# Kernel tuning notes

Measured on AMD Instinct MI355X. Metric: run time of the kernel, lower is better.

The kernel has to match this reference:

```python
import jax, jax.numpy as jnp
import numpy as np
from jax import lax

N_FFT = 1024
HOP = 256
FFT_BIN = N_FFT // 2 + 1  # 513


def make_stft_kernel(n_fft: int) -> jnp.ndarray:
    """Fixed DFT basis kernel, shape (2*fft_bin, 1, n_fft), windowed with periodic Hann."""
    fft_bin = n_fft // 2 + 1
    # torch.linspace(0, 1, n_fft) is endpoint-inclusive, same as jnp.linspace
    t = jnp.linspace(0.0, 1.0, n_fft, dtype=jnp.float32)[None, None, :]
    k = jnp.arange(fft_bin, dtype=jnp.float32)[:, None, None]
    xt = t * k * (2.0 * jnp.pi)
    kernel = jnp.concatenate([jnp.cos(xt), jnp.sin(xt)], axis=0)  # (2*fft_bin, 1, n_fft)
    # torch.hann_window is periodic: 0.5*(1 - cos(2*pi*n/N))
    n = jnp.arange(n_fft, dtype=jnp.float32)
    hann = 0.5 * (1.0 - jnp.cos(2.0 * jnp.pi * n / n_fft))
    return kernel * hann[None, None, :]


def setup_inputs() -> dict:
    key = jax.random.key(0)
    x = jax.random.normal(key, (16, 1, 262144), dtype=jnp.float32)
    kernel = make_stft_kernel(N_FFT)
    return {"x": x, "kernel": kernel}


def reference(x, kernel):
    # padding == 'center'
    left = N_FFT // 2
    right = N_FFT - left
    x = jnp.pad(x, ((0, 0), (0, 0), (left, right)))
    # strided conv1d with fixed DFT-basis kernel
    y = lax.conv_general_dilated(
        x, kernel,
        window_strides=(HOP,),
        padding='VALID',
        dimension_numbers=('NCW', 'OIW', 'NCW'),
    )  # (B, 2*fft_bin, num_frames)
    real, imag = jnp.split(y, 2, axis=1)
    return real, imag
```

## Files before the change

kernel.cpp:

```cpp
#include <hip/hip_runtime.h>
#include <hip/hip_bf16.h>

#define NFFT    1024
#define HOPSZ   256
#define XLEN    262144
#define PADLEN  (XLEN + NFFT)
#define NBATCH  16
#define NBINS2  1026
#define FBIN    513
#define NFRAMES 1025
#define NGF     (NBATCH * NFRAMES)
#define TOTOUT  ((size_t)NBATCH * FBIN * NFRAMES)

#define KT 64
#define NKT 16
#define NT_TILES 64
#define MT_TILES 4
#define NWG (MT_TILES * NT_TILES)
#define ABYTES 32768
#define BUFE   32768
#define BUFB   65536
#define NTAIL  49184
#define PSTRIDE 132
#define LDS_BYTES (256 * PSTRIDE * 4)

typedef short bf16x8 __attribute__((ext_vector_type(8)));
typedef float f32x4  __attribute__((ext_vector_type(4)));
typedef unsigned short u16x8 __attribute__((ext_vector_type(8)));
typedef unsigned short u16x4 __attribute__((ext_vector_type(4)));

__device__ __forceinline__ unsigned short f2bf(float f) {
  union { float f; unsigned u; } v; v.f = f;
  unsigned r = v.u + 0x7fffu + ((v.u >> 16) & 1u);
  return (unsigned short)(r >> 16);
}
__device__ __forceinline__ float bf2f(unsigned short h) {
  union { unsigned u; float f; } v; v.u = ((unsigned)h) << 16; return v.f;
}

typedef __attribute__((address_space(1))) void void_g;
typedef __attribute__((address_space(3))) void void_l;
__device__ __forceinline__ void gload_lds16(const void* g, void* l) {
  __builtin_amdgcn_global_load_lds((void_g*)(g), (void_l*)(l), 16, 0, 0);
}

__global__ __launch_bounds__(256) void pack_x_kernel(const float* __restrict__ x,
                                                     unsigned short* __restrict__ xp) {
  long long t = (long long)blockIdx.x * 256 + threadIdx.x;
  long long base = t * 8;
  if (base >= (long long)NBATCH * PADLEN) return;
  int b   = (int)(base / PADLEN);
  int pos = (int)(base % PADLEN);
  const float* xb = x + (long long)b * XLEN;
  u16x8 v;
#pragma unroll
  for (int j = 0; j < 8; ++j) {
    int xi = pos + j - (NFFT / 2);
    float f = ((unsigned)xi < (unsigned)XLEN) ? xb[xi] : 0.0f;
    v[j] = f2bf(f);
  }
  *reinterpret_cast<u16x8*>(xp + base) = v;
}

__global__ __launch_bounds__(256) void pack_w_kernel(const float* __restrict__ W,
                                                     unsigned short* __restrict__ Wb) {
  long long t = ((long long)blockIdx.x * 256 + threadIdx.x) * 4;
  if (t >= (long long)NBINS2 * NFFT) return;
  float4 f = *reinterpret_cast<const float4*>(W + t);
  u16x4 v;
  v[0] = f2bf(f.x); v[1] = f2bf(f.y); v[2] = f2bf(f.z); v[3] = f2bf(f.w);
  *reinterpret_cast<u16x4*>(Wb + t) = v;
}

__global__ __launch_bounds__(512, 2) void stft_mfma8_kernel(const unsigned short* __restrict__ Xp,
                                                            const unsigned short* __restrict__ Wb,
                                                            float* __restrict__ out) {
  extern __shared__ unsigned short lds[];
  const int tid = threadIdx.x;
  const int l   = tid & 63;
  const int w   = tid >> 6;
  const int wr  = w >> 2;
  const int wc  = w & 3;
  const int r16 = l & 15, hi = l >> 4;

  const int bid = blockIdx.x;
  const int c_  = bid >> 3;
  const int nt  = (bid & 7) * 8 + (c_ & 7);
  const int mt  = c_ >> 3;
  const int bin0 = mt * 256;
  const int gf0  = nt * 256;

  const int lr = l >> 3;
  const int ls = l & 7;
  const int cswz = ((ls ^ lr) << 3);

  unsigned aqoff[4];
#pragma unroll
  for (int qi = 0; qi < 4; ++qi)
    aqoff[qi] = (unsigned)(bin0 + qi * 64 + w * 8 + lr) * NFFT + cswz;
  unsigned boff[4];
#pragma unroll
  for (int j = 0; j < 4; ++j) {
    const int gf = gf0 + (w * 4 + j) * 8 + lr;
    const int bb = gf / NFRAMES;
    const int fr = gf - bb * NFRAMES;
    boff[j] = (unsigned)bb * PADLEN + (unsigned)fr * HOPSZ + cswz;
  }

#define STAGE(D, KC) do { \
    _Pragma("unroll") \
    for (int q_ = 0; q_ < 4; ++q_) \
      gload_lds16(Wb + aqoff[q_] + (KC), lds + (D) * BUFE + q_ * 4096 + w * 512); \
    _Pragma("unroll") \
    for (int j_ = 0; j_ < 4; ++j_) \
      gload_lds16(Xp + boff[j_] + (KC), lds + (D) * BUFE + 16384 + (w * 4 + j_) * 512); \
    } while (0)

  const int aB0 = (wr * 128 + r16) * 128;
  const int bB0 = ABYTES + (wc * 64 + r16) * 128;
  const int swz = (r16 & 7) << 4;
  const int c0  = (hi * 16) ^ swz;
  const int c1  = (64 + hi * 16) ^ swz;

#define RD12(BASE, C, AARR, BARR) do { \
    _Pragma("unroll") \
    for (int n_ = 0; n_ < 4; ++n_) \
      BARR[n_] = *reinterpret_cast<const bf16x8*>((const char*)(BASE) + bB0 + n_ * 2048 + (C)); \
    _Pragma("unroll") \
    for (int m_ = 0; m_ < 8; ++m_) \
      AARR[m_] = *reinterpret_cast<const bf16x8*>((const char*)(BASE) + aB0 + m_ * 2048 + (C)); \
    } while (0)

#define MFMA32(AARR, BARR) do { \
    __builtin_amdgcn_s_setprio(1); \
    _Pragma("unroll") \
    for (int m_ = 0; m_ < 8; ++m_) { \
      _Pragma("unroll") \
      for (int n_ = 0; n_ < 4; ++n_) \
        acc[m_][n_] = __builtin_amdgcn_mfma_f32_16x16x32_bf16(AARR[m_], BARR[n_], acc[m_][n_], 0, 0, 0); \
    } \
    __builtin_amdgcn_s_setprio(0); } while (0)

  f32x4 acc[8][4] = {};
  bf16x8 A0[8], B0[4], A1[8], B1[4];

  STAGE(0, 0);
  STAGE(1, KT);
  asm volatile("s_waitcnt vmcnt(8)" ::: "memory");
  __builtin_amdgcn_s_barrier();
  __builtin_amdgcn_sched_barrier(0);
  RD12(lds, c0, A0, B0);

  for (int t = 0; t < NKT; ++t) {
    const int ci = t & 1;
    const char* cbuf = (const char*)lds + ci * BUFB;
    const char* nbuf = (const char*)lds + (ci ^ 1) * BUFB;
    const int kc2 = (t + 2) << 6;

    RD12(cbuf, c1, A1, B1);
    __builtin_amdgcn_sched_barrier(0);
    asm volatile("s_waitcnt lgkmcnt(12)" ::: "memory");
    __builtin_amdgcn_sched_barrier(0);
    MFMA32(A0, B0);

    asm volatile("s_waitcnt vmcnt(0) lgkmcnt(0)" ::: "memory");
    __builtin_amdgcn_sched_barrier(0);
    __builtin_amdgcn_s_barrier();
    __builtin_amdgcn_sched_barrier(0);
    if (t < NKT - 1) RD12(nbuf, c0, A0, B0);
    if (t < NKT - 2) STAGE(ci, kc2);
    __builtin_amdgcn_sched_barrier(0);
    MFMA32(A1, B1);
  }

  {
    float* patch = (float*)lds;
    const int col     = l & 15;
    const int rbase   = (l >> 4) * 4;
    const int h_mine  = wc >> 1;
    const int colbase = (wc & 1) * 64;

#pragma unroll
    for (int h = 0; h < 2; ++h) {
      __builtin_amdgcn_s_barrier();
      if (h_mine == h) {
#pragma unroll
        for (int m = 0; m < 8; ++m)
#pragma unroll
          for (int n2 = 0; n2 < 4; ++n2)
#pragma unroll
            for (int r = 0; r < 4; ++r)
              patch[(wr * 128 + m * 16 + rbase + r) * PSTRIDE + colbase + n2 * 16 + col] =
                  acc[m][n2][r];
      }
      __builtin_amdgcn_s_barrier();

      size_t baseR[2];
      int cols[2];
#pragma unroll
      for (int j = 0; j < 2; ++j) {
        const int gf = gf0 + h * 128 + j * 64 + l;
        const int bb = gf / NFRAMES;
        const int fr = gf - bb * NFRAMES;
        baseR[j] = (size_t)bb * FBIN * NFRAMES + fr;
        cols[j]  = j * 64 + l;
      }
      for (int i = 0; i < 32; ++i) {
        const int row = i * 8 + w;
        const int bin = bin0 + row;
        const size_t binoff = (size_t)bin * NFRAMES;
#pragma unroll
        for (int j = 0; j < 2; ++j) {
          const float v = patch[row * PSTRIDE + cols[j]];
          size_t off = binoff + (bin < FBIN ? baseR[j]
                                            : baseR[j] + TOTOUT - (size_t)FBIN * NFRAMES);
          out[off] = v;
        }
      }
    }
  }
#undef STAGE
#undef RD12
#undef MFMA32
}

__global__ __launch_bounds__(512) void stft_tail_kernel(const unsigned short* __restrict__ Xp,
                                                        const unsigned short* __restrict__ Wb,
                                                        float* __restrict__ out) {
  const int wid = (int)((blockIdx.x * 512 + threadIdx.x) >> 6);
  const int l   = threadIdx.x & 63;
  if (wid >= NTAIL) return;
  int bin, gf;
  if (wid < 2 * NGF) { bin = 1024 + (wid & 1); gf = wid >> 1; }
  else { const int s = wid - 2 * NGF; gf = 16384 + (s & 15); bin = s >> 4; }
  const int bb = gf / NFRAMES;
  const int fr = gf - bb * NFRAMES;
  const unsigned short* xr = Xp + (size_t)bb * PADLEN + (size_t)fr * HOPSZ + l * 16;
  const unsigned short* wr = Wb + (size_t)bin * NFFT + l * 16;
  u16x8 x0 = *reinterpret_cast<const u16x8*>(xr);
  u16x8 x1 = *reinterpret_cast<const u16x8*>(xr + 8);
  u16x8 w0 = *reinterpret_cast<const u16x8*>(wr);
  u16x8 w1 = *reinterpret_cast<const u16x8*>(wr + 8);
  float s0 = 0.f, s1 = 0.f;
#pragma unroll
  for (int j = 0; j < 8; ++j) {
    s0 = fmaf(bf2f(x0[j]), bf2f(w0[j]), s0);
    s1 = fmaf(bf2f(x1[j]), bf2f(w1[j]), s1);
  }
  float s = s0 + s1;
#pragma unroll
  for (int k = 32; k >= 1; k >>= 1) s += __shfl_xor(s, k);
  if (l == 0) {
    size_t off;
    if (bin < FBIN) off = ((size_t)bb * FBIN + bin) * NFRAMES + fr;
    else            off = TOTOUT + ((size_t)bb * FBIN + (bin - FBIN)) * NFRAMES + fr;
    out[off] = s;
  }
}

__global__ void stft_direct_kernel(const float* __restrict__ x, const float* __restrict__ W,
                                   float* __restrict__ out,
                                   int bin_lo, int nbins, int fr_lo, int nframes) {
  long long total = (long long)NBATCH * nbins * nframes;
  for (long long t = (long long)blockIdx.x * blockDim.x + threadIdx.x; t < total;
       t += (long long)gridDim.x * blockDim.x) {
    int fr = fr_lo + (int)(t % nframes);
    long long q = t / nframes;
    int bin = bin_lo + (int)(q % nbins);
    int b   = (int)(q / nbins);
    const float* xb = x + (long long)b * XLEN;
    const float* wrow = W + (long long)bin * NFFT;
    float s = 0.f;
    const int base = fr * HOPSZ - (NFFT / 2);
    for (int j = 0; j < NFFT; ++j) {
      int xi = base + j;
      float xv = ((unsigned)xi < (unsigned)XLEN) ? xb[xi] : 0.f;
      s = fmaf(xv, wrow[j], s);
    }
    size_t off;
    if (bin < FBIN) off = ((size_t)b * FBIN + bin) * NFRAMES + fr;
    else            off = TOTOUT + ((size_t)b * FBIN + (bin - FBIN)) * NFRAMES + fr;
    out[off] = s;
  }
}

extern "C" void kernel_launch(void* const* d_in, const int* in_sizes, int n_in,
                              void* d_out, int out_size, void* d_ws, size_t ws_size,
                              hipStream_t stream) {
  const float* x = (const float*)d_in[0];
  const float* W = (const float*)d_in[1];
  float* out = (float*)d_out;

  const size_t xp_bytes = (size_t)NBATCH * PADLEN * sizeof(unsigned short);
  const size_t wb_bytes = (size_t)NBINS2 * NFFT * sizeof(unsigned short);

  if (ws_size >= xp_bytes + wb_bytes) {
    unsigned short* xp = (unsigned short*)d_ws;
    unsigned short* wb = (unsigned short*)((char*)d_ws + xp_bytes);

    {
      long long threads = (long long)NBATCH * PADLEN / 8;
      pack_x_kernel<<<(int)((threads + 255) / 256), 256, 0, stream>>>(x, xp);
    }
    pack_w_kernel<<<(NBINS2 * NFFT / 4 + 255) / 256, 256, 0, stream>>>(W, wb);

    stft_mfma8_kernel<<<NWG, 512, LDS_BYTES, stream>>>(xp, wb, out);
    stft_tail_kernel<<<NTAIL / 8, 512, 0, stream>>>(xp, wb, out);
  } else {
    stft_direct_kernel<<<2048, 256, 0, stream>>>(x, W, out, 0, NBINS2, 0, NFRAMES);
  }
}
```

Baseline: 69.39 us.

## Restructure GEMM main loop into quadrant-wise LDS reads and MFMA phases

Replaces the two-half K-split software pipeline (RD12/MFMA32 with depth-2 prefetch) with a four-phase quadrant schedule. Each phase reads only the A or B fragments it needs and issues 16 MFMAs on one 4x2 accumulator quadrant, with workgroup barriers between phases. Global prefetch depth drops from two stages ahead to one, and the loop is no longer unrolled. The aim is to interleave LDS reads with MFMA work across waves, HipKittens-style, and to lower register pressure. The extra barriers and shallower prefetch may expose more global-load latency.

```diff
diff --git a/kernel.cpp b/kernel.cpp
--- a/kernel.cpp
+++ b/kernel.cpp
@@ -122,55 +122,80 @@
   const int c0  = (hi * 16) ^ swz;
   const int c1  = (64 + hi * 16) ^ swz;
 
-#define RD12(BASE, C, AARR, BARR) do { \
-    _Pragma("unroll") \
-    for (int n_ = 0; n_ < 4; ++n_) \
-      BARR[n_] = *reinterpret_cast<const bf16x8*>((const char*)(BASE) + bB0 + n_ * 2048 + (C)); \
-    _Pragma("unroll") \
-    for (int m_ = 0; m_ < 8; ++m_) \
-      AARR[m_] = *reinterpret_cast<const bf16x8*>((const char*)(BASE) + aB0 + m_ * 2048 + (C)); \
-    } while (0)
-
-#define MFMA32(AARR, BARR) do { \
+#define RD_A(CB, MH, AARR) do { \
+    _Pragma("unroll") \
+    for (int m_ = 0; m_ < 4; ++m_) { \
+      AARR[m_ * 2 + 0] = *reinterpret_cast<const bf16x8*>((CB) + aB0 + ((MH) * 4 + m_) * 2048 + c0); \
+      AARR[m_ * 2 + 1] = *reinterpret_cast<const bf16x8*>((CB) + aB0 + ((MH) * 4 + m_) * 2048 + c1); \
+    } } while (0)
+#define RD_B(CB, NH, BARR) do { \
+    _Pragma("unroll") \
+    for (int n_ = 0; n_ < 2; ++n_) { \
+      BARR[n_ * 2 + 0] = *reinterpret_cast<const bf16x8*>((CB) + bB0 + ((NH) * 2 + n_) * 2048 + c0); \
+      BARR[n_ * 2 + 1] = *reinterpret_cast<const bf16x8*>((CB) + bB0 + ((NH) * 2 + n_) * 2048 + c1); \
+    } } while (0)
+
+#define MFMA_Q(AARR, BARR, MH, NH) do { \
     __builtin_amdgcn_s_setprio(1); \
     _Pragma("unroll") \
-    for (int m_ = 0; m_ < 8; ++m_) { \
+    for (int m_ = 0; m_ < 4; ++m_) { \
       _Pragma("unroll") \
-      for (int n_ = 0; n_ < 4; ++n_) \
-        acc[m_][n_] = __builtin_amdgcn_mfma_f32_16x16x32_bf16(AARR[m_], BARR[n_], acc[m_][n_], 0, 0, 0); \
+      for (int n_ = 0; n_ < 2; ++n_) { \
+        acc[(MH) * 4 + m_][(NH) * 2 + n_] = __builtin_amdgcn_mfma_f32_16x16x32_bf16( \
+            AARR[m_ * 2 + 0], BARR[n_ * 2 + 0], acc[(MH) * 4 + m_][(NH) * 2 + n_], 0, 0, 0); \
+        acc[(MH) * 4 + m_][(NH) * 2 + n_] = __builtin_amdgcn_mfma_f32_16x16x32_bf16( \
+            AARR[m_ * 2 + 1], BARR[n_ * 2 + 1], acc[(MH) * 4 + m_][(NH) * 2 + n_], 0, 0, 0); \
+      } \
     } \
     __builtin_amdgcn_s_setprio(0); } while (0)
 
+#define LGKM0  asm volatile("s_waitcnt lgkmcnt(0)" ::: "memory"); __builtin_amdgcn_sched_barrier(0)
+#define SBAR   __builtin_amdgcn_s_barrier()
+#define SCHED0 __builtin_amdgcn_sched_barrier(0)
+
   f32x4 acc[8][4] = {};
-  bf16x8 A0[8], B0[4], A1[8], B1[4];
+  bf16x8 Am0[8], Am1[8], Bn0[4], Bn1[4];
 
   STAGE(0, 0);
-  STAGE(1, KT);
-  asm volatile("s_waitcnt vmcnt(8)" ::: "memory");
-  __builtin_amdgcn_s_barrier();
-  __builtin_amdgcn_sched_barrier(0);
-  RD12(lds, c0, A0, B0);
-
+  asm volatile("s_waitcnt vmcnt(0)" ::: "memory");
+  SCHED0;
+  SBAR;
+  SCHED0;
+
+#pragma unroll 1
   for (int t = 0; t < NKT; ++t) {
-    const int ci = t & 1;
-    const char* cbuf = (const char*)lds + ci * BUFB;
-    const char* nbuf = (const char*)lds + (ci ^ 1) * BUFB;
-    const int kc2 = (t + 2) << 6;
-
-    RD12(cbuf, c1, A1, B1);
-    __builtin_amdgcn_sched_barrier(0);
-    asm volatile("s_waitcnt lgkmcnt(12)" ::: "memory");
-    __builtin_amdgcn_sched_barrier(0);
-    MFMA32(A0, B0);
-
-    asm volatile("s_waitcnt vmcnt(0) lgkmcnt(0)" ::: "memory");
-    __builtin_amdgcn_sched_barrier(0);
-    __builtin_amdgcn_s_barrier();
-    __builtin_amdgcn_sched_barrier(0);
-    if (t < NKT - 1) RD12(nbuf, c0, A0, B0);
-    if (t < NKT - 2) STAGE(ci, kc2);
-    __builtin_amdgcn_sched_barrier(0);
-    MFMA32(A1, B1);
+    const char* cbuf = (const char*)lds + (t & 1) * BUFB;
+    const int kc1 = (t + 1) << 6;
+
+    RD_A(cbuf, 0, Am0);
+    RD_B(cbuf, 0, Bn0);
+    SCHED0;
+    if (t < NKT - 1) STAGE((t & 1) ^ 1, kc1);
+    SBAR;
+    LGKM0;
+    MFMA_Q(Am0, Bn0, 0, 0);
+    SBAR;
+
+    RD_A(cbuf, 1, Am1);
+    SCHED0;
+    SBAR;
+    LGKM0;
+    MFMA_Q(Am1, Bn0, 1, 0);
+    SBAR;
+
+    RD_B(cbuf, 1, Bn1);
+    SCHED0;
+    SBAR;
+    LGKM0;
+    MFMA_Q(Am1, Bn1, 1, 1);
+    SBAR;
+
+    MFMA_Q(Am0, Bn1, 0, 1);
+    if (t < NKT - 1) {
+      asm volatile("s_waitcnt vmcnt(0)" ::: "memory");
+      SCHED0;
+    }
+    SBAR;
   }
 
   {
@@ -182,7 +207,7 @@
 
 #pragma unroll
     for (int h = 0; h < 2; ++h) {
-      __builtin_amdgcn_s_barrier();
+      SBAR;
       if (h_mine == h) {
 #pragma unroll
         for (int m = 0; m < 8; ++m)
@@ -193,7 +218,7 @@
               patch[(wr * 128 + m * 16 + rbase + r) * PSTRIDE + colbase + n2 * 16 + col] =
                   acc[m][n2][r];
       }
-      __builtin_amdgcn_s_barrier();
+      SBAR;
 
       size_t baseR[2];
       int cols[2];
@@ -220,8 +245,12 @@
     }
   }
 #undef STAGE
-#undef RD12
-#undef MFMA32
+#undef RD_A
+#undef RD_B
+#undef MFMA_Q
+#undef LGKM0
+#undef SBAR
+#undef SCHED0
 }
 
 __global__ __launch_bounds__(512) void stft_tail_kernel(const unsigned short* __restrict__ Xp,
```

Result: slower. 72.81 us (+4.9%).

## Fuse pack and tail kernels into one prep launch, store MFMA results directly

Applied to the files above, without the earlier changes.

Merges the x/W bf16 packing kernels and the tail-bin kernel into a single prep kernel. The tail part now reads fp32 inputs directly, so it no longer waits on the packed buffers, and launch count drops from four to two. The MFMA kernel swaps operand roles so each accumulator's four lanes map to consecutive frames. Each thread then writes a 4-wide vector straight to global memory, removing the LDS transpose staging and its barriers. The tail now uses fp32 rather than bf16 math, and the direct stores have less coalescing across lanes than the old row-wise writes.

```diff
diff --git a/kernel.cpp b/kernel.cpp
--- a/kernel.cpp
+++ b/kernel.cpp
@@ -21,11 +21,16 @@
 #define BUFE   32768
 #define BUFB   65536
 #define NTAIL  49184
-#define PSTRIDE 132
-#define LDS_BYTES (256 * PSTRIDE * 4)
+#define LDS_BYTES (2 * BUFB)
+
+#define PX_BLKS 2056
+#define PW_BLKS 1026
+#define TL_BLKS 12296
+#define PREP_BLKS (PX_BLKS + PW_BLKS + TL_BLKS)
 
 typedef short bf16x8 __attribute__((ext_vector_type(8)));
 typedef float f32x4  __attribute__((ext_vector_type(4)));
+typedef float f32x4u __attribute__((ext_vector_type(4), aligned(4)));
 typedef unsigned short u16x8 __attribute__((ext_vector_type(8)));
 typedef unsigned short u16x4 __attribute__((ext_vector_type(4)));
 
@@ -34,9 +39,6 @@
   unsigned r = v.u + 0x7fffu + ((v.u >> 16) & 1u);
   return (unsigned short)(r >> 16);
 }
-__device__ __forceinline__ float bf2f(unsigned short h) {
-  union { unsigned u; float f; } v; v.u = ((unsigned)h) << 16; return v.f;
-}
 
 typedef __attribute__((address_space(1))) void void_g;
 typedef __attribute__((address_space(3))) void void_l;
@@ -44,32 +46,74 @@
   __builtin_amdgcn_global_load_lds((void_g*)(g), (void_l*)(l), 16, 0, 0);
 }
 
-__global__ __launch_bounds__(256) void pack_x_kernel(const float* __restrict__ x,
-                                                     unsigned short* __restrict__ xp) {
-  long long t = (long long)blockIdx.x * 256 + threadIdx.x;
-  long long base = t * 8;
-  if (base >= (long long)NBATCH * PADLEN) return;
-  int b   = (int)(base / PADLEN);
-  int pos = (int)(base % PADLEN);
-  const float* xb = x + (long long)b * XLEN;
-  u16x8 v;
-#pragma unroll
-  for (int j = 0; j < 8; ++j) {
-    int xi = pos + j - (NFFT / 2);
-    float f = ((unsigned)xi < (unsigned)XLEN) ? xb[xi] : 0.0f;
-    v[j] = f2bf(f);
-  }
-  *reinterpret_cast<u16x8*>(xp + base) = v;
-}
-
-__global__ __launch_bounds__(256) void pack_w_kernel(const float* __restrict__ W,
-                                                     unsigned short* __restrict__ Wb) {
-  long long t = ((long long)blockIdx.x * 256 + threadIdx.x) * 4;
-  if (t >= (long long)NBINS2 * NFFT) return;
-  float4 f = *reinterpret_cast<const float4*>(W + t);
-  u16x4 v;
-  v[0] = f2bf(f.x); v[1] = f2bf(f.y); v[2] = f2bf(f.z); v[3] = f2bf(f.w);
-  *reinterpret_cast<u16x4*>(Wb + t) = v;
+__global__ __launch_bounds__(256) void prep_kernel(const float* __restrict__ x,
+                                                   const float* __restrict__ W,
+                                                   unsigned short* __restrict__ xp,
+                                                   unsigned short* __restrict__ wb,
+                                                   float* __restrict__ out) {
+  const int bid = blockIdx.x;
+  const int tid = threadIdx.x;
+
+  if (bid < PX_BLKS) {
+    long long base = ((long long)bid * 256 + tid) * 8;
+    int b   = (int)(base / PADLEN);
+    int pos = (int)(base % PADLEN);
+    const float* xb = x + (long long)b * XLEN;
+    u16x8 v;
+#pragma unroll
+    for (int j = 0; j < 8; ++j) {
+      int xi = pos + j - (NFFT / 2);
+      float f = ((unsigned)xi < (unsigned)XLEN) ? xb[xi] : 0.0f;
+      v[j] = f2bf(f);
+    }
+    *reinterpret_cast<u16x8*>(xp + base) = v;
+    return;
+  }
+  if (bid < PX_BLKS + PW_BLKS) {
+    long long t = (((long long)(bid - PX_BLKS)) * 256 + tid) * 4;
+    float4 f = *reinterpret_cast<const float4*>(W + t);
+    u16x4 v;
+    v[0] = f2bf(f.x); v[1] = f2bf(f.y); v[2] = f2bf(f.z); v[3] = f2bf(f.w);
+    *reinterpret_cast<u16x4*>(wb + t) = v;
+    return;
+  }
+  {
+    const int wid = (bid - PX_BLKS - PW_BLKS) * 4 + (tid >> 6);
+    const int l   = tid & 63;
+    int bin, gf;
+    if (wid < 2 * NGF) { bin = 1024 + (wid & 1); gf = wid >> 1; }
+    else { const int s = wid - 2 * NGF; gf = 16384 + (s & 15); bin = s >> 4; }
+    const int bb = gf / NFRAMES;
+    const int fr = gf - bb * NFRAMES;
+    const float* xb = x + (size_t)bb * XLEN;
+    const float* wrow = W + (size_t)bin * NFFT + l * 16;
+    const int base = fr * HOPSZ - (NFFT / 2) + l * 16;
+    float s0 = 0.f;
+    if (fr >= 2 && fr <= 1022) {
+#pragma unroll
+      for (int q = 0; q < 4; ++q) {
+        float4 xv = *reinterpret_cast<const float4*>(xb + base + q * 4);
+        float4 wv = *reinterpret_cast<const float4*>(wrow + q * 4);
+        s0 = fmaf(xv.x, wv.x, s0); s0 = fmaf(xv.y, wv.y, s0);
+        s0 = fmaf(xv.z, wv.z, s0); s0 = fmaf(xv.w, wv.w, s0);
+      }
+    } else {
+#pragma unroll
+      for (int j = 0; j < 16; ++j) {
+        int xi = base + j;
+        float xv = ((unsigned)xi < (unsigned)XLEN) ? xb[xi] : 0.f;
+        s0 = fmaf(xv, wrow[j], s0);
+      }
+    }
+#pragma unroll
+    for (int k = 32; k >= 1; k >>= 1) s0 += __shfl_xor(s0, k);
+    if (l == 0) {
+      size_t off;
+      if (bin < FBIN) off = ((size_t)bb * FBIN + bin) * NFRAMES + fr;
+      else            off = TOTOUT + ((size_t)bb * FBIN + (bin - FBIN)) * NFRAMES + fr;
+      out[off] = s0;
+    }
+  }
 }
 
 __global__ __launch_bounds__(512, 2) void stft_mfma8_kernel(const unsigned short* __restrict__ Xp,
@@ -116,105 +160,91 @@
       gload_lds16(Xp + boff[j_] + (KC), lds + (D) * BUFE + 16384 + (w * 4 + j_) * 512); \
     } while (0)
 
-  const int aB0 = (wr * 128 + r16) * 128;
-  const int bB0 = ABYTES + (wc * 64 + r16) * 128;
+  const int xB0 = ABYTES + (wr * 128 + r16) * 128;
+  const int wB0 = (wc * 64 + r16) * 128;
   const int swz = (r16 & 7) << 4;
   const int c0  = (hi * 16) ^ swz;
   const int c1  = (64 + hi * 16) ^ swz;
 
-#define RD12(BASE, C, AARR, BARR) do { \
+#define RD12(BASE, C, XARR, WARR) do { \
     _Pragma("unroll") \
     for (int n_ = 0; n_ < 4; ++n_) \
-      BARR[n_] = *reinterpret_cast<const bf16x8*>((const char*)(BASE) + bB0 + n_ * 2048 + (C)); \
+      WARR[n_] = *reinterpret_cast<const bf16x8*>((const char*)(BASE) + wB0 + n_ * 2048 + (C)); \
     _Pragma("unroll") \
     for (int m_ = 0; m_ < 8; ++m_) \
-      AARR[m_] = *reinterpret_cast<const bf16x8*>((const char*)(BASE) + aB0 + m_ * 2048 + (C)); \
+      XARR[m_] = *reinterpret_cast<const bf16x8*>((const char*)(BASE) + xB0 + m_ * 2048 + (C)); \
     } while (0)
 
-#define MFMA32(AARR, BARR) do { \
+#define MFMA32(XARR, WARR) do { \
     __builtin_amdgcn_s_setprio(1); \
     _Pragma("unroll") \
     for (int m_ = 0; m_ < 8; ++m_) { \
       _Pragma("unroll") \
       for (int n_ = 0; n_ < 4; ++n_) \
-        acc[m_][n_] = __builtin_amdgcn_mfma_f32_16x16x32_bf16(AARR[m_], BARR[n_], acc[m_][n_], 0, 0, 0); \
+        acc[m_][n_] = __builtin_amdgcn_mfma_f32_16x16x32_bf16(XARR[m_], WARR[n_], acc[m_][n_], 0, 0, 0); \
     } \
     __builtin_amdgcn_s_setprio(0); } while (0)
 
   f32x4 acc[8][4] = {};
-  bf16x8 A0[8], B0[4], A1[8], B1[4];
+  bf16x8 X0[8], W0[4], X1[8], W1[4];
 
   STAGE(0, 0);
   STAGE(1, KT);
   asm volatile("s_waitcnt vmcnt(8)" ::: "memory");
   __builtin_amdgcn_s_barrier();
   __builtin_amdgcn_sched_barrier(0);
-  RD12(lds, c0, A0, B0);
-
+  RD12(lds, c0, X0, W0);
+
+#pragma unroll 1
   for (int t = 0; t < NKT; ++t) {
     const int ci = t & 1;
     const char* cbuf = (const char*)lds + ci * BUFB;
     const char* nbuf = (const char*)lds + (ci ^ 1) * BUFB;
     const int kc2 = (t + 2) << 6;
 
-    RD12(cbuf, c1, A1, B1);
+    RD12(cbuf, c1, X1, W1);
     __builtin_amdgcn_sched_barrier(0);
     asm volatile("s_waitcnt lgkmcnt(12)" ::: "memory");
     __builtin_amdgcn_sched_barrier(0);
-    MFMA32(A0, B0);
+    MFMA32(X0, W0);
 
     asm volatile("s_waitcnt vmcnt(0) lgkmcnt(0)" ::: "memory");
     __builtin_amdgcn_sched_barrier(0);
     __builtin_amdgcn_s_barrier();
     __builtin_amdgcn_sched_barrier(0);
-    if (t < NKT - 1) RD12(nbuf, c0, A0, B0);
+    if (t < NKT - 1) RD12(nbuf, c0, X0, W0);
     if (t < NKT - 2) STAGE(ci, kc2);
     __builtin_amdgcn_sched_barrier(0);
-    MFMA32(A1, B1);
+    MFMA32(X1, W1);
   }
 
   {
-    float* patch = (float*)lds;
-    const int col     = l & 15;
-    const int rbase   = (l >> 4) * 4;
-    const int h_mine  = wc >> 1;
-    const int colbase = (wc & 1) * 64;
-
-#pragma unroll
-    for (int h = 0; h < 2; ++h) {
-      __builtin_amdgcn_s_barrier();
-      if (h_mine == h) {
-#pragma unroll
-        for (int m = 0; m < 8; ++m)
-#pragma unroll
-          for (int n2 = 0; n2 < 4; ++n2)
-#pragma unroll
-            for (int r = 0; r < 4; ++r)
-              patch[(wr * 128 + m * 16 + rbase + r) * PSTRIDE + colbase + n2 * 16 + col] =
-                  acc[m][n2][r];
-      }
-      __builtin_amdgcn_s_barrier();
-
-      size_t baseR[2];
-      int cols[2];
-#pragma unroll
-      for (int j = 0; j < 2; ++j) {
-        const int gf = gf0 + h * 128 + j * 64 + l;
-        const int bb = gf / NFRAMES;
-        const int fr = gf - bb * NFRAMES;
-        baseR[j] = (size_t)bb * FBIN * NFRAMES + fr;
-        cols[j]  = j * 64 + l;
-      }
-      for (int i = 0; i < 32; ++i) {
-        const int row = i * 8 + w;
-        const int bin = bin0 + row;
-        const size_t binoff = (size_t)bin * NFRAMES;
-#pragma unroll
-        for (int j = 0; j < 2; ++j) {
-          const float v = patch[row * PSTRIDE + cols[j]];
-          size_t off = binoff + (bin < FBIN ? baseR[j]
-                                            : baseR[j] + TOTOUT - (size_t)FBIN * NFRAMES);
-          out[off] = v;
+    const int bcol  = l & 15;
+    const int fquad = (l >> 4) * 4;
+#pragma unroll
+    for (int mf = 0; mf < 8; ++mf) {
+      const int gf = gf0 + wr * 128 + mf * 16 + fquad;
+      const int bb = gf / NFRAMES;
+      const int fr = gf - bb * NFRAMES;
+#pragma unroll
+      for (int nb = 0; nb < 4; ++nb) {
+        const int bin = bin0 + wc * 64 + nb * 16 + bcol;
+        if (fr <= NFRAMES - 4) {
+          size_t rowbase;
+          if (bin < FBIN) rowbase = ((size_t)bb * FBIN + bin) * NFRAMES;
+          else            rowbase = TOTOUT + ((size_t)bb * FBIN + (bin - FBIN)) * NFRAMES;
+          *reinterpret_cast<f32x4u*>(out + rowbase + fr) = acc[mf][nb];
+        } else {
+#pragma unroll
+          for (int r = 0; r < 4; ++r) {
+            const int gfr = gf + r;
+            const int bbr = gfr / NFRAMES;
+            const int frr = gfr - bbr * NFRAMES;
+            size_t rb;
+            if (bin < FBIN) rb = ((size_t)bbr * FBIN + bin) * NFRAMES;
+            else            rb = TOTOUT + ((size_t)bbr * FBIN + (bin - FBIN)) * NFRAMES;
+            out[rb + frr] = acc[mf][nb][r];
+          }
         }
       }
     }
@@ -222,40 +252,6 @@
 #undef STAGE
 #undef RD12
 #undef MFMA32
-}
-
-__global__ __launch_bounds__(512) void stft_tail_kernel(const unsigned short* __restrict__ Xp,
-                                                        const unsigned short* __restrict__ Wb,
-                                                        float* __restrict__ out) {
-  const int wid = (int)((blockIdx.x * 512 + threadIdx.x) >> 6);
-  const int l   = threadIdx.x & 63;
-  if (wid >= NTAIL) return;
-  int bin, gf;
-  if (wid < 2 * NGF) { bin = 1024 + (wid & 1); gf = wid >> 1; }
-  else { const int s = wid - 2 * NGF; gf = 16384 + (s & 15); bin = s >> 4; }
-  const int bb = gf / NFRAMES;
-  const int fr = gf - bb * NFRAMES;
-  const unsigned short* xr = Xp + (size_t)bb * PADLEN + (size_t)fr * HOPSZ + l * 16;
-  const unsigned short* wr = Wb + (size_t)bin * NFFT + l * 16;
-  u16x8 x0 = *reinterpret_cast<const u16x8*>(xr);
-  u16x8 x1 = *reinterpret_cast<const u16x8*>(xr + 8);
-  u16x8 w0 = *reinterpret_cast<const u16x8*>(wr);
-  u16x8 w1 = *reinterpret_cast<const u16x8*>(wr + 8);
-  float s0 = 0.f, s1 = 0.f;
-#pragma unroll
-  for (int j = 0; j < 8; ++j) {
-    s0 = fmaf(bf2f(x0[j]), bf2f(w0[j]), s0);
-    s1 = fmaf(bf2f(x1[j]), bf2f(w1[j]), s1);
-  }
-  float s = s0 + s1;
-#pragma unroll
-  for (int k = 32; k >= 1; k >>= 1) s += __shfl_xor(s, k);
-  if (l == 0) {
-    size_t off;
-    if (bin < FBIN) off = ((size_t)bb * FBIN + bin) * NFRAMES + fr;
-    else            off = TOTOUT + ((size_t)bb * FBIN + (bin - FBIN)) * NFRAMES + fr;
-    out[off] = s;
-  }
 }
 
 __global__ void stft_direct_kernel(const float* __restrict__ x, const float* __restrict__ W,
@@ -298,14 +294,8 @@
     unsigned short* xp = (unsigned short*)d_ws;
     unsigned short* wb = (unsigned short*)((char*)d_ws + xp_bytes);
 
-    {
-      long long threads = (long long)NBATCH * PADLEN / 8;
-      pack_x_kernel<<<(int)((threads + 255) / 256), 256, 0, stream>>>(x, xp);
-    }
-    pack_w_kernel<<<(NBINS2 * NFFT / 4 + 255) / 256, 256, 0, stream>>>(W, wb);
-
+    prep_kernel<<<PREP_BLKS, 256, 0, stream>>>(x, W, xp, wb, out);
     stft_mfma8_kernel<<<NWG, 512, LDS_BYTES, stream>>>(xp, wb, out);
-    stft_tail_kernel<<<NTAIL / 8, 512, 0, stream>>>(xp, wb, out);
   } else {
     stft_direct_kernel<<<2048, 256, 0, stream>>>(x, W, out, 0, NBINS2, 0, NFRAMES);
   }
```

After: 95.96 us. +38.3%, slower.

## Retile STFT GEMM to 256x128 tiles with 4 waves and triple-buffered K=32 staging

Applied to the files above, without the earlier changes.

Replaces the 8-wave 256x256-tile GEMM kernel with a 4-wave 256x128-tile kernel. It stages K in chunks of 32 through a three-deep LDS ring, so one barrier per step overlaps loads with MFMA work. The frame-major epilogue now writes two adjacent frames per lane as 8-byte stores, with special handling where a pair crosses a batch boundary. The aim is to double the workgroup count, improve occupancy, shrink LDS use and widen output stores, at the cost of less data reuse per tile and more K iterations.

```diff
diff --git a/kernel.cpp b/kernel.cpp
--- a/kernel.cpp
+++ b/kernel.cpp
@@ -12,20 +12,18 @@
 #define NGF     (NBATCH * NFRAMES)
 #define TOTOUT  ((size_t)NBATCH * FBIN * NFRAMES)
 
-#define KT 64
-#define NKT 16
-#define NT_TILES 64
-#define MT_TILES 4
-#define NWG (MT_TILES * NT_TILES)
-#define ABYTES 32768
-#define BUFE   32768
-#define BUFB   65536
+#define KT 32
+#define NKT 32
+#define NWG 512
+#define BUFE 12288
+#define BUFB 24576
+#define LDS_BYTES (3 * BUFB)
 #define NTAIL  49184
 #define PSTRIDE 132
-#define LDS_BYTES (256 * PSTRIDE * 4)
 
 typedef short bf16x8 __attribute__((ext_vector_type(8)));
 typedef float f32x4  __attribute__((ext_vector_type(4)));
+typedef float f32x2u __attribute__((ext_vector_type(2), aligned(4)));
 typedef unsigned short u16x8 __attribute__((ext_vector_type(8)));
 typedef unsigned short u16x4 __attribute__((ext_vector_type(4)));
 
@@ -72,149 +70,153 @@
   *reinterpret_cast<u16x4*>(Wb + t) = v;
 }
 
-__global__ __launch_bounds__(512, 2) void stft_mfma8_kernel(const unsigned short* __restrict__ Xp,
+__global__ __launch_bounds__(256, 2) void stft_mfma4_kernel(const unsigned short* __restrict__ Xp,
                                                             const unsigned short* __restrict__ Wb,
                                                             float* __restrict__ out) {
   extern __shared__ unsigned short lds[];
   const int tid = threadIdx.x;
   const int l   = tid & 63;
   const int w   = tid >> 6;
-  const int wr  = w >> 2;
-  const int wc  = w & 3;
   const int r16 = l & 15, hi = l >> 4;
 
-  const int bid = blockIdx.x;
-  const int c_  = bid >> 3;
-  const int nt  = (bid & 7) * 8 + (c_ & 7);
-  const int mt  = c_ >> 3;
+  const int bid  = blockIdx.x;
+  const int wgid = (bid & 7) * 64 + (bid >> 3);
+  const int mt   = wgid >> 7;
+  const int nt   = wgid & 127;
   const int bin0 = mt * 256;
-  const int gf0  = nt * 256;
-
-  const int lr = l >> 3;
-  const int ls = l & 7;
-  const int cswz = ((ls ^ lr) << 3);
+  const int gf0  = nt * 128;
+
+  const int lr = l >> 2;
+  const int ls = l & 3;
+  const int gsw = (lr >> 1) & 3;
+  const int cswz = ((ls ^ gsw) << 3);
 
   unsigned aqoff[4];
 #pragma unroll
-  for (int qi = 0; qi < 4; ++qi)
-    aqoff[qi] = (unsigned)(bin0 + qi * 64 + w * 8 + lr) * NFFT + cswz;
-  unsigned boff[4];
-#pragma unroll
-  for (int j = 0; j < 4; ++j) {
-    const int gf = gf0 + (w * 4 + j) * 8 + lr;
+  for (int qq = 0; qq < 4; ++qq)
+    aqoff[qq] = (unsigned)(bin0 + w * 64 + qq * 16 + lr) * NFFT + cswz;
+  unsigned boff[2];
+#pragma unroll
+  for (int jj = 0; jj < 2; ++jj) {
+    const int gf = gf0 + w * 32 + jj * 16 + lr;
     const int bb = gf / NFRAMES;
     const int fr = gf - bb * NFRAMES;
-    boff[j] = (unsigned)bb * PADLEN + (unsigned)fr * HOPSZ + cswz;
+    boff[jj] = (unsigned)bb * PADLEN + (unsigned)fr * HOPSZ + cswz;
   }
 
 #define STAGE(D, KC) do { \
     _Pragma("unroll") \
     for (int q_ = 0; q_ < 4; ++q_) \
-      gload_lds16(Wb + aqoff[q_] + (KC), lds + (D) * BUFE + q_ * 4096 + w * 512); \
-    _Pragma("unroll") \
-    for (int j_ = 0; j_ < 4; ++j_) \
-      gload_lds16(Xp + boff[j_] + (KC), lds + (D) * BUFE + 16384 + (w * 4 + j_) * 512); \
+      gload_lds16(Wb + aqoff[q_] + (KC), lds + (D) * BUFE + (w * 4 + q_) * 512); \
+    _Pragma("unroll") \
+    for (int j_ = 0; j_ < 2; ++j_) \
+      gload_lds16(Xp + boff[j_] + (KC), lds + (D) * BUFE + 8192 + (w * 2 + j_) * 512); \
     } while (0)
 
-  const int aB0 = (wr * 128 + r16) * 128;
-  const int bB0 = ABYTES + (wc * 64 + r16) * 128;
-  const int swz = (r16 & 7) << 4;
-  const int c0  = (hi * 16) ^ swz;
-  const int c1  = (64 + hi * 16) ^ swz;
-
-#define RD12(BASE, C, AARR, BARR) do { \
+  const int swzb  = ((hi ^ ((r16 >> 1) & 3)) << 4);
+  const int wbase = (w * 64 + r16) * 64 + swzb;
+  const int xbase = 16384 + r16 * 64 + swzb;
+
+#define RD12(DOFF, WARR, XARR) do { \
     _Pragma("unroll") \
     for (int n_ = 0; n_ < 4; ++n_) \
-      BARR[n_] = *reinterpret_cast<const bf16x8*>((const char*)(BASE) + bB0 + n_ * 2048 + (C)); \
+      WARR[n_] = *reinterpret_cast<const bf16x8*>((const char*)lds + (DOFF) + wbase + n_ * 1024); \
     _Pragma("unroll") \
     for (int m_ = 0; m_ < 8; ++m_) \
-      AARR[m_] = *reinterpret_cast<const bf16x8*>((const char*)(BASE) + aB0 + m_ * 2048 + (C)); \
+      XARR[m_] = *reinterpret_cast<const bf16x8*>((const char*)lds + (DOFF) + xbase + m_ * 1024); \
     } while (0)
 
-#define MFMA32(AARR, BARR) do { \
+#define MFMA32(WARR, XARR) do { \
     __builtin_amdgcn_s_setprio(1); \
     _Pragma("unroll") \
-    for (int m_ = 0; m_ < 8; ++m_) { \
+    for (int a_ = 0; a_ < 4; ++a_) { \
       _Pragma("unroll") \
-      for (int n_ = 0; n_ < 4; ++n_) \
-        acc[m_][n_] = __builtin_amdgcn_mfma_f32_16x16x32_bf16(AARR[m_], BARR[n_], acc[m_][n_], 0, 0, 0); \
+      for (int b_ = 0; b_ < 8; ++b_) \
+        acc[a_][b_] = __builtin_amdgcn_mfma_f32_16x16x32_bf16(WARR[a_], XARR[b_], acc[a_][b_], 0, 0, 0); \
     } \
     __builtin_amdgcn_s_setprio(0); } while (0)
 
-  f32x4 acc[8][4] = {};
-  bf16x8 A0[8], B0[4], A1[8], B1[4];
+#define ITER(NXTB, STGB, WIN, XIN, WOUT, XOUT) do { \
+    RD12((NXTB) * BUFB, WOUT, XOUT); \
+    __builtin_amdgcn_sched_barrier(0); \
+    STAGE(STGB, kc); kc += KT; \
+    asm volatile("s_waitcnt lgkmcnt(12)" ::: "memory"); \
+    __builtin_amdgcn_sched_barrier(0); \
+    MFMA32(WIN, XIN); \
+    asm volatile("s_waitcnt vmcnt(0)" ::: "memory"); \
+    __builtin_amdgcn_sched_barrier(0); \
+    __builtin_amdgcn_s_barrier(); \
+    __builtin_amdgcn_sched_barrier(0); \
+    } while (0)
+
+  f32x4 acc[4][8] = {};
+  bf16x8 WA[4], XA[8], WB[4], XB[8];
 
   STAGE(0, 0);
   STAGE(1, KT);
-  asm volatile("s_waitcnt vmcnt(8)" ::: "memory");
+  asm volatile("s_waitcnt vmcnt(0)" ::: "memory");
+  __builtin_amdgcn_sched_barrier(0);
   __builtin_amdgcn_s_barrier();
   __builtin_amdgcn_sched_barrier(0);
-  RD12(lds, c0, A0, B0);
-
-  for (int t = 0; t < NKT; ++t) {
-    const int ci = t & 1;
-    const char* cbuf = (const char*)lds + ci * BUFB;
-    const char* nbuf = (const char*)lds + (ci ^ 1) * BUFB;
-    const int kc2 = (t + 2) << 6;
-
-    RD12(cbuf, c1, A1, B1);
-    __builtin_amdgcn_sched_barrier(0);
-    asm volatile("s_waitcnt lgkmcnt(12)" ::: "memory");
-    __builtin_amdgcn_sched_barrier(0);
-    MFMA32(A0, B0);
-
-    asm volatile("s_waitcnt vmcnt(0) lgkmcnt(0)" ::: "memory");
-    __builtin_amdgcn_sched_barrier(0);
-    __builtin_amdgcn_s_barrier();
-    __builtin_amdgcn_sched_barrier(0);
-    if (t < NKT - 1) RD12(nbuf, c0, A0, B0);
-    if (t < NKT - 2) STAGE(ci, kc2);
-    __builtin_amdgcn_sched_barrier(0);
-    MFMA32(A1, B1);
-  }
+  RD12(0, WA, XA);
+
+  int kc = 2 * KT;
+#pragma unroll 1
+  for (int g = 0; g < 5; ++g) {
+    ITER(1, 2, WA, XA, WB, XB);
+    ITER(2, 0, WB, XB, WA, XA);
+    ITER(0, 1, WA, XA, WB, XB);
+    ITER(1, 2, WB, XB, WA, XA);
+    ITER(2, 0, WA, XA, WB, XB);
+    ITER(0, 1, WB, XB, WA, XA);
+  }
+  RD12(1 * BUFB, WB, XB);
+  asm volatile("s_waitcnt lgkmcnt(12)" ::: "memory");
+  __builtin_amdgcn_sched_barrier(0);
+  MFMA32(WA, XA);
+  asm volatile("s_waitcnt lgkmcnt(0)" ::: "memory");
+  __builtin_amdgcn_sched_barrier(0);
+  MFMA32(WB, XB);
 
   {
     float* patch = (float*)lds;
-    const int col     = l & 15;
-    const int rbase   = (l >> 4) * 4;
-    const int h_mine  = wc >> 1;
-    const int colbase = (wc & 1) * 64;
-
-#pragma unroll
-    for (int h = 0; h < 2; ++h) {
+    const int col   = l & 15;
+    const int rbase = (l >> 4) * 4;
+    const int gfE = gf0 + 2 * l;
+    const int bbE = gfE / NFRAMES;
+    const int frE = gfE - bbE * NFRAMES;
+    const bool split = (frE == 1024);
+
+#pragma unroll 1
+    for (int c = 0; c < 4; ++c) {
       __builtin_amdgcn_s_barrier();
-      if (h_mine == h) {
-#pragma unroll
-        for (int m = 0; m < 8; ++m)
-#pragma unroll
-          for (int n2 = 0; n2 < 4; ++n2)
+      if (w == c) {
+#pragma unroll
+        for (int a = 0; a < 4; ++a)
+#pragma unroll
+          for (int b = 0; b < 8; ++b)
 #pragma unroll
             for (int r = 0; r < 4; ++r)
-              patch[(wr * 128 + m * 16 + rbase + r) * PSTRIDE + colbase + n2 * 16 + col] =
-                  acc[m][n2][r];
+              patch[(a * 16 + rbase + r) * PSTRIDE + b * 16 + col] = acc[a][b][r];
       }
       __builtin_amdgcn_s_barrier();
 
-      size_t baseR[2];
-      int cols[2];
-#pragma unroll
-      for (int j = 0; j < 2; ++j) {
-        const int gf = gf0 + h * 128 + j * 64 + l;
-        const int bb = gf / NFRAMES;
-        const int fr = gf - bb * NFRAMES;
-        baseR[j] = (size_t)bb * FBIN * NFRAMES + fr;
-        cols[j]  = j * 64 + l;
-      }
-      for (int i = 0; i < 32; ++i) {
-        const int row = i * 8 + w;
-        const int bin = bin0 + row;
-        const size_t binoff = (size_t)bin * NFRAMES;
-#pragma unroll
-        for (int j = 0; j < 2; ++j) {
-          const float v = patch[row * PSTRIDE + cols[j]];
-          size_t off = binoff + (bin < FBIN ? baseR[j]
-                                            : baseR[j] + TOTOUT - (size_t)FBIN * NFRAMES);
-          out[off] = v;
+#pragma unroll
+      for (int i = 0; i < 16; ++i) {
+        const int row = i * 4 + w;
+        const int bin = bin0 + c * 64 + row;
+        f32x2u v = *reinterpret_cast<const f32x2u*>(patch + row * PSTRIDE + 2 * l);
+        size_t rowbase;
+        if (bin < FBIN) rowbase = ((size_t)bbE * FBIN + bin) * NFRAMES;
+        else            rowbase = TOTOUT + ((size_t)bbE * FBIN + (bin - FBIN)) * NFRAMES;
+        if (!split) {
+          *reinterpret_cast<f32x2u*>(out + rowbase + frE) = v;
+        } else {
+          size_t rowbase2;
+          if (bin < FBIN) rowbase2 = ((size_t)(bbE + 1) * FBIN + bin) * NFRAMES;
+          else            rowbase2 = TOTOUT + ((size_t)(bbE + 1) * FBIN + (bin - FBIN)) * NFRAMES;
+          out[rowbase + 1024] = v[0];
+          out[rowbase2]       = v[1];
         }
       }
     }
@@ -222,6 +224,7 @@
 #undef STAGE
 #undef RD12
 #undef MFMA32
+#undef ITER
 }
 
 __global__ __launch_bounds__(512) void stft_tail_kernel(const unsigned short* __restrict__ Xp,
@@ -304,7 +307,7 @@
     }
     pack_w_kernel<<<(NBINS2 * NFFT / 4 + 255) / 256, 256, 0, stream>>>(W, wb);
 
-    stft_mfma8_kernel<<<NWG, 512, LDS_BYTES, stream>>>(xp, wb, out);
+    stft_mfma4_kernel<<<NWG, 256, LDS_BYTES, stream>>>(xp, wb, out);
     stft_tail_kernel<<<NTAIL / 8, 512, 0, stream>>>(xp, wb, out);
   } else {
     stft_direct_kernel<<<2048, 256, 0, stream>>>(x, W, out, 0, NBINS2, 0, NFRAMES);
```

Measured after the change: 83.06 us. 1.2x slower.
